# Optimization experiments

Measured on AMD Instinct MI355X. Metric: run time of the kernel, lower is better.

The kernel has to match this reference:

```python
import jax, jax.numpy as jnp
import numpy as np

N = 50000      # nodes
E = 800000     # edges (before self loops)
F_IN = 128     # input feature dim
H = 4          # attention heads
C = 64         # per-head channels (hidden_dim = out_channels = 64)
HC = H * C     # 256, concat output width of each GATv2Conv
G = 32         # number of graphs in the batch
NEG_SLOPE_ATT = 0.2   # GATv2 internal LeakyReLU
NEG_SLOPE_ACT = 0.01  # encoder nn.LeakyReLU() default


def _glorot(key, shape, fan_in):
    return jax.random.normal(key, shape, jnp.float32) * (1.0 / np.sqrt(fan_in))


def setup_inputs() -> dict:
    key = jax.random.key(0)
    ks = jax.random.split(key, 32)
    inp = {}
    inp["x"] = jax.random.normal(ks[0], (N, F_IN), jnp.float32)
    inp["edge_index"] = jax.random.randint(ks[1], (2, E), 0, N, jnp.int32)
    inp["batch"] = jnp.sort(jax.random.randint(ks[2], (N,), 0, G, jnp.int32))
    i = 3
    for li, fin in ((1, F_IN), (2, HC), (3, HC)):
        inp[f"Wl{li}"] = _glorot(ks[i], (HC, fin), fin); i += 1
        inp[f"bl{li}"] = jnp.zeros((HC,), jnp.float32)
        inp[f"Wr{li}"] = _glorot(ks[i], (HC, fin), fin); i += 1
        inp[f"br{li}"] = jnp.zeros((HC,), jnp.float32)
        inp[f"att{li}"] = _glorot(ks[i], (H, C), C); i += 1
        inp[f"bo{li}"] = jnp.zeros((HC,), jnp.float32)
    return inp


def _gatv2_layer(x, src, dst, Wl, bl, Wr, br, att, bo):
    n = x.shape[0]
    xl = (x @ Wl.T + bl).reshape(n, H, C)  # source transform
    xr = (x @ Wr.T + br).reshape(n, H, C)  # target transform
    # per-edge attention logits: a^T LeakyReLU(xl[j] + xr[i])
    e = jax.nn.leaky_relu(xl[src] + xr[dst], negative_slope=NEG_SLOPE_ATT)  # [E', H, C]
    score = jnp.einsum('ehc,hc->eh', e, att)                                # [E', H]
    # segment softmax over incoming edges of each destination node
    m = jax.ops.segment_max(score, dst, num_segments=n)
    p = jnp.exp(score - m[dst])
    s = jax.ops.segment_sum(p, dst, num_segments=n)
    alpha = p / s[dst]
    out = jax.ops.segment_sum(alpha[:, :, None] * xl[src], dst, num_segments=n)
    return out.reshape(n, HC) + bo


def reference(x, edge_index, batch,
              Wl1, bl1, Wr1, br1, att1, bo1,
              Wl2, bl2, Wr2, br2, att2, bo2,
              Wl3, bl3, Wr3, br3, att3, bo3):
    loop = jnp.arange(N, dtype=edge_index.dtype)
    src = jnp.concatenate([edge_index[0], loop])  # add self loops (PyG default)
    dst = jnp.concatenate([edge_index[1], loop])
    h = _gatv2_layer(x, src, dst, Wl1, bl1, Wr1, br1, att1, bo1)
    h = jax.nn.leaky_relu(h, negative_slope=NEG_SLOPE_ACT)
    h = _gatv2_layer(h, src, dst, Wl2, bl2, Wr2, br2, att2, bo2)
    h = jax.nn.leaky_relu(h, negative_slope=NEG_SLOPE_ACT)
    h = _gatv2_layer(h, src, dst, Wl3, bl3, Wr3, br3, att3, bo3)
    # global mean pool over graphs
    sums = jax.ops.segment_sum(h, batch, num_segments=G)
    cnt = jax.ops.segment_sum(jnp.ones((N,), h.dtype), batch, num_segments=G)
    return sums / jnp.maximum(cnt, 1.0)[:, None]
```

## Files before the change

### kernel.cpp

```cpp
#include <hip/hip_runtime.h>

#define HEADS 4
#define CH 64
#define HC 256
#define NGRAPH 32
#define NEG_ATT 0.2f
#define NEG_ACT 0.01f

typedef __attribute__((ext_vector_type(8))) short bf16x8;
typedef __attribute__((ext_vector_type(4))) float f32x4;
typedef __attribute__((ext_vector_type(2))) float f32x2;

typedef __attribute__((address_space(3))) unsigned int lds_u32;
typedef const __attribute__((address_space(1))) unsigned int glob_u32;

__device__ __forceinline__ void gl_lds16(const void* g, void* l) {
  __builtin_amdgcn_global_load_lds((glob_u32*)(uintptr_t)g,
                                   (lds_u32*)(unsigned int)(uintptr_t)l, 16, 0, 0);
}

__device__ __forceinline__ void split2(float a, float b, unsigned& hi, unsigned& lo) {
  unsigned ua = __float_as_uint(a), ub = __float_as_uint(b);
  float la = a - __uint_as_float(ua & 0xFFFF0000u);
  float lb = b - __uint_as_float(ub & 0xFFFF0000u);
  hi = __builtin_amdgcn_perm(ub, ua, 0x07060302u);
  lo = __builtin_amdgcn_perm(__float_as_uint(lb), __float_as_uint(la), 0x07060302u);
}

__device__ __forceinline__ unsigned rtn_bf16(float f) {
  unsigned u = __float_as_uint(f);
  return (u + 0x7FFFu + ((u >> 16) & 1u)) >> 16;
}
__device__ __forceinline__ unsigned rtn_pack2(float a, float b) {
  return (rtn_bf16(b) << 16) | rtn_bf16(a);
}

__global__ __launch_bounds__(256) void convert_x(
    const float* __restrict__ X, unsigned short* __restrict__ xhi,
    unsigned short* __restrict__ xlo, int total4) {
  int g = blockIdx.x * 256 + threadIdx.x;
  if (g >= total4) return;
  float4 v = *(const float4*)&X[(size_t)g * 4];
  uint2 h2, l2;
  split2(v.x, v.y, h2.x, l2.x);
  split2(v.z, v.w, h2.y, l2.y);
  *(uint2*)&xhi[(size_t)g * 4] = h2;
  *(uint2*)&xlo[(size_t)g * 4] = l2;
}

__device__ __forceinline__ void conv_w_one(
    int g, const float* Wl, const float* Wr, int K,
    unsigned short* wfhi, unsigned short* wflo) {
  int lane = g & 63;
  int ct = (g >> 6) & 31;
  int kb = g >> 11;
  int col = ct * 16 + (lane & 15);
  int k = kb * 32 + (lane >> 4) * 8;
  const float* src = (col < HC) ? &Wl[(size_t)col * K + k] : &Wr[(size_t)(col - HC) * K + k];
  float4 v0 = *(const float4*)src;
  float4 v1 = *(const float4*)(src + 4);
  uint4 hq, lq;
  split2(v0.x, v0.y, hq.x, lq.x);
  split2(v0.z, v0.w, hq.y, lq.y);
  split2(v1.x, v1.y, hq.z, lq.z);
  split2(v1.z, v1.w, hq.w, lq.w);
  *(uint4*)&wfhi[(size_t)g * 8] = hq;
  *(uint4*)&wflo[(size_t)g * 8] = lq;
}

__global__ __launch_bounds__(256) void convert_w_all(
    const float* __restrict__ Wl1, const float* __restrict__ Wr1,
    unsigned short* __restrict__ w1hi, unsigned short* __restrict__ w1lo,
    const float* __restrict__ Wl2, const float* __restrict__ Wr2,
    unsigned short* __restrict__ w2hi, unsigned short* __restrict__ w2lo,
    const float* __restrict__ Wl3, const float* __restrict__ Wr3,
    unsigned short* __restrict__ w3hi, unsigned short* __restrict__ w3lo) {
  int g = blockIdx.x * 256 + threadIdx.x;
  if (g < 8192) conv_w_one(g, Wl1, Wr1, 128, w1hi, w1lo);
  else if (g < 8192 + 16384) conv_w_one(g - 8192, Wl2, Wr2, 256, w2hi, w2lo);
  else conv_w_one(g - 8192 - 16384, Wl3, Wr3, 256, w3hi, w3lo);
}

template <int K>
__global__ __launch_bounds__(256) void gemm_fused(
    const unsigned short* __restrict__ xhi, const unsigned short* __restrict__ xlo,
    const unsigned short* __restrict__ wfhi, const unsigned short* __restrict__ wflo,
    const float* __restrict__ bl, const float* __restrict__ br,
    unsigned short* __restrict__ Y1, unsigned short* __restrict__ Y2, int N, int nrb) {
  constexpr int nkb = K >> 5;
  __shared__ unsigned short Ah[2][128][32];
  __shared__ unsigned short Al[2][128][32];

  const int f = blockIdx.x;
  const int rb = (f & 7) + 8 * (f >> 5);
  const int cb = (f >> 3) & 3;
  if (rb >= nrb) return;

  const int tid = threadIdx.x;
  const int wave = tid >> 6;
  const int lane = tid & 63;
  const int quad = lane >> 4;
  const int l16 = lane & 15;
  const int wr = (wave >> 1) * 64;
  const int wc = (wave & 1) * 64;
  const int row0 = rb * 128;
  const int col0 = cb * 128;
  const int ctg0 = cb * 8 + (wave & 1) * 4;

  const int c0 = tid, c1 = tid + 256;
  const int r0g = row0 + (c0 >> 2), r1g = row0 + (c1 >> 2);
  const int ko0 = (c0 & 3) * 8, ko1 = (c1 & 3) * 8;
  const int gr0 = (r0g < N) ? r0g : N - 1;
  const int gr1 = (r1g < N) ? r1g : N - 1;

  f32x4 acc[4][4];
#pragma unroll
  for (int i = 0; i < 4; i++)
#pragma unroll
    for (int j = 0; j < 4; j++) acc[i][j] = (f32x4){0.f, 0.f, 0.f, 0.f};

  {
    size_t ga0 = (size_t)gr0 * K + ko0;
    size_t ga1 = (size_t)gr1 * K + ko1;
    gl_lds16(&xhi[ga0], &Ah[0][c0 >> 2][ko0]);
    gl_lds16(&xlo[ga0], &Al[0][c0 >> 2][ko0]);
    gl_lds16(&xhi[ga1], &Ah[0][c1 >> 2][ko1]);
    gl_lds16(&xlo[ga1], &Al[0][c1 >> 2][ko1]);
  }

#pragma unroll
  for (int kb = 0; kb < nkb; kb++) {
    const int cur = kb & 1, nxt = cur ^ 1;
    bf16x8 bhi[4], blo[4];
#pragma unroll
    for (int j = 0; j < 4; j++) {
      size_t ci = ((size_t)kb * 32 + ctg0 + j) * 64 + lane;
      bhi[j] = *(const bf16x8*)&wfhi[ci * 8];
      blo[j] = *(const bf16x8*)&wflo[ci * 8];
    }
    __syncthreads();
    if (kb + 1 < nkb) {
      int k0 = (kb + 1) * 32;
      size_t ga0 = (size_t)gr0 * K + k0 + ko0;
      size_t ga1 = (size_t)gr1 * K + k0 + ko1;
      gl_lds16(&xhi[ga0], &Ah[nxt][c0 >> 2][ko0]);
      gl_lds16(&xlo[ga0], &Al[nxt][c0 >> 2][ko0]);
      gl_lds16(&xhi[ga1], &Ah[nxt][c1 >> 2][ko1]);
      gl_lds16(&xlo[ga1], &Al[nxt][c1 >> 2][ko1]);
    }
    bf16x8 ahi[4], alo[4];
#pragma unroll
    for (int i = 0; i < 4; i++) {
      ahi[i] = *(const bf16x8*)&Ah[cur][wr + i * 16 + l16][quad * 8];
      alo[i] = *(const bf16x8*)&Al[cur][wr + i * 16 + l16][quad * 8];
    }
#pragma unroll
    for (int i = 0; i < 4; i++)
#pragma unroll
      for (int j = 0; j < 4; j++) {
        acc[i][j] = __builtin_amdgcn_mfma_f32_16x16x32_bf16(ahi[i], bhi[j], acc[i][j], 0, 0, 0);
        acc[i][j] = __builtin_amdgcn_mfma_f32_16x16x32_bf16(ahi[i], blo[j], acc[i][j], 0, 0, 0);
        acc[i][j] = __builtin_amdgcn_mfma_f32_16x16x32_bf16(alo[i], bhi[j], acc[i][j], 0, 0, 0);
      }
  }

#pragma unroll
  for (int j = 0; j < 4; j++) {
    int colg = col0 + wc + j * 16 + l16;
    unsigned short* Yp = (colg < HC) ? Y1 : Y2;
    int cc = (colg < HC) ? colg : colg - HC;
    float bv = (colg < HC) ? bl[cc] : br[cc];
#pragma unroll
    for (int i = 0; i < 4; i++)
#pragma unroll
      for (int r = 0; r < 4; r++) {
        int row = row0 + wr + i * 16 + quad * 4 + r;
        if (row < N)
          Yp[(size_t)row * HC + cc] = (unsigned short)rtn_bf16(acc[i][j][r] + bv);
      }
  }
}

__global__ __launch_bounds__(256) void hist_dst(
    const int* __restrict__ edst, int* __restrict__ counts, int E) {
  int e = blockIdx.x * 256 + threadIdx.x;
  if (e < E) atomicAdd(&counts[edst[e]], 1);
}

__global__ __launch_bounds__(256) void scan_blocks(
    const int* __restrict__ counts, int* __restrict__ row_start,
    int* __restrict__ bsum, int N) {
  __shared__ int tmp[256];
  int t = threadIdx.x;
  int base = blockIdx.x * 1024 + t * 4;
  int v0 = (base     < N) ? counts[base]     + 1 : 0;
  int v1 = (base + 1 < N) ? counts[base + 1] + 1 : 0;
  int v2 = (base + 2 < N) ? counts[base + 2] + 1 : 0;
  int v3 = (base + 3 < N) ? counts[base + 3] + 1 : 0;
  int c1 = v0 + v1, c2 = c1 + v2, tot = c2 + v3;
  tmp[t] = tot;
  __syncthreads();
  for (int off = 1; off < 256; off <<= 1) {
    int add = (t >= off) ? tmp[t - off] : 0;
    __syncthreads();
    tmp[t] += add;
    __syncthreads();
  }
  int excl = tmp[t] - tot;
  if (base     < N) row_start[base + 1] = excl + v0;
  if (base + 1 < N) row_start[base + 2] = excl + c1;
  if (base + 2 < N) row_start[base + 3] = excl + c2;
  if (base + 3 < N) row_start[base + 4] = excl + tot;
  if (t == 255) bsum[blockIdx.x] = tmp[255];
  if (blockIdx.x == 0 && t == 0) row_start[0] = 0;
}

__global__ void scan_tops(int* __restrict__ bsum, int nb) {
  int lane = threadIdx.x;
  int v = (lane < nb) ? bsum[lane] : 0;
  for (int off = 1; off < 64; off <<= 1) {
    int u = __shfl_up(v, off);
    if (lane >= off) v += u;
  }
  if (lane < nb) bsum[lane] = v;
}

__global__ __launch_bounds__(256) void scan_add(
    int* __restrict__ row_start, const int* __restrict__ bsum, int N) {
  int off = bsum[blockIdx.x];
  int i = (blockIdx.x + 1) * 1024 + threadIdx.x * 4;
#pragma unroll
  for (int k = 0; k < 4; k++)
    if (i + k < N) row_start[i + k + 1] += off;
}

__global__ __launch_bounds__(256) void csr_init(
    const int* __restrict__ row_start, int* __restrict__ fill_pos,
    int* __restrict__ csr_src, int N) {
  int i = blockIdx.x * 256 + threadIdx.x;
  if (i < N) {
    int p = row_start[i];
    csr_src[p] = i << 9;
    fill_pos[i] = p + 1;
  }
}

__global__ __launch_bounds__(256) void csr_scatter(
    const int* __restrict__ esrc, const int* __restrict__ edst,
    int* __restrict__ fill_pos, int* __restrict__ csr_src, int E) {
  int e = blockIdx.x * 256 + threadIdx.x;
  if (e < E) {
    int p = atomicAdd(&fill_pos[edst[e]], 1);
    csr_src[p] = esrc[e] << 9;
  }
}

__device__ __forceinline__ void unpk(uint2 q, f32x2& v01, f32x2& v23) {
  v01.x = __uint_as_float(q.x << 16);
  v01.y = __uint_as_float(q.x & 0xFFFF0000u);
  v23.x = __uint_as_float(q.y << 16);
  v23.y = __uint_as_float(q.y & 0xFFFF0000u);
}

__device__ __forceinline__ float edot(f32x2 l01, f32x2 l23, f32x2 r01, f32x2 r23,
                                      f32x2 a01, f32x2 a23) {
  f32x2 t01 = l01 + r01, t23 = l23 + r23;
  f32x2 u01 = t01 * NEG_ATT, u23 = t23 * NEG_ATT;
  t01.x = fmaxf(t01.x, u01.x); t01.y = fmaxf(t01.y, u01.y);
  t23.x = fmaxf(t23.x, u23.x); t23.y = fmaxf(t23.y, u23.y);
  f32x2 dv = t01 * a01 + t23 * a23;
  float d = dv.x + dv.y;
  d += __shfl_xor(d, 1);
  d += __shfl_xor(d, 2);
  d += __shfl_xor(d, 4);
  d += __shfl_xor(d, 8);
  return d;
}

__global__ __launch_bounds__(256) void gat_fused(
    const unsigned short* __restrict__ xl, const unsigned short* __restrict__ xr,
    const int* __restrict__ row_start, const int* __restrict__ csr_soff,
    const float* __restrict__ att, const float* __restrict__ bo,
    unsigned short* __restrict__ ohi, unsigned short* __restrict__ olo,
    int N, int mode) {
  int dst = (blockIdx.x * 256 + threadIdx.x) >> 6;
  int lane = threadIdx.x & 63;
  if (dst >= N) return;
  int h = lane >> 4;
  int off = h * CH + (lane & 15) * 4;
  const int loff = off * 2;
  const char* xlc = (const char*)xl;
  f32x2 a01 = *(const f32x2*)&att[off];
  f32x2 a23 = *(const f32x2*)&att[off + 2];
  f32x2 r01, r23;
  unpk(*(const uint2*)&xr[(size_t)dst * HC + off], r01, r23);
  f32x2 o01 = {0.f, 0.f}, o23 = {0.f, 0.f};
  float s = 0.f;
  int p = row_start[dst];
  int end = row_start[dst + 1];
  for (; p + 4 <= end; p += 4) {
    int b0 = csr_soff[p + 0] + loff, b1 = csr_soff[p + 1] + loff;
    int b2 = csr_soff[p + 2] + loff, b3 = csr_soff[p + 3] + loff;
    uint2 q0 = *(const uint2*)(xlc + b0);
    uint2 q1 = *(const uint2*)(xlc + b1);
    uint2 q2 = *(const uint2*)(xlc + b2);
    uint2 q3 = *(const uint2*)(xlc + b3);
    f32x2 l0a, l0b, l1a, l1b, l2a, l2b, l3a, l3b;
    unpk(q0, l0a, l0b);
    unpk(q1, l1a, l1b);
    unpk(q2, l2a, l2b);
    unpk(q3, l3a, l3b);
    float e0 = __expf(edot(l0a, l0b, r01, r23, a01, a23));
    float e1 = __expf(edot(l1a, l1b, r01, r23, a01, a23));
    float e2 = __expf(edot(l2a, l2b, r01, r23, a01, a23));
    float e3 = __expf(edot(l3a, l3b, r01, r23, a01, a23));
    s += (e0 + e1) + (e2 + e3);
    o01 = l0a * e0 + o01;
    o01 = l1a * e1 + o01;
    o01 = l2a * e2 + o01;
    o01 = l3a * e3 + o01;
    o23 = l0b * e0 + o23;
    o23 = l1b * e1 + o23;
    o23 = l2b * e2 + o23;
    o23 = l3b * e3 + o23;
  }
  for (; p < end; p++) {
    int b0 = csr_soff[p] + loff;
    uint2 q0 = *(const uint2*)(xlc + b0);
    f32x2 la, lb;
    unpk(q0, la, lb);
    float pe = __expf(edot(la, lb, r01, r23, a01, a23));
    s += pe;
    o01 = la * pe + o01;
    o23 = lb * pe + o23;
  }
  float inv = 1.f / s;
  f32x2 b01 = *(const f32x2*)&bo[off];
  f32x2 b23 = *(const f32x2*)&bo[off + 2];
  f32x2 res01 = o01 * inv + b01;
  f32x2 res23 = o23 * inv + b23;
  if (mode == 1) {
    f32x2 v01 = res01 * NEG_ACT, v23 = res23 * NEG_ACT;
    res01.x = fmaxf(res01.x, v01.x); res01.y = fmaxf(res01.y, v01.y);
    res23.x = fmaxf(res23.x, v23.x); res23.y = fmaxf(res23.y, v23.y);
    uint2 h2, l2;
    split2(res01.x, res01.y, h2.x, l2.x);
    split2(res23.x, res23.y, h2.y, l2.y);
    *(uint2*)&ohi[(size_t)dst * HC + off] = h2;
    *(uint2*)&olo[(size_t)dst * HC + off] = l2;
  } else {
    uint2 pk;
    pk.x = rtn_pack2(res01.x, res01.y);
    pk.y = rtn_pack2(res23.x, res23.y);
    *(uint2*)&ohi[(size_t)dst * HC + off] = pk;
  }
}

__global__ __launch_bounds__(256) void pool_partial(
    const unsigned short* __restrict__ h3, const int* __restrict__ batch,
    float* __restrict__ out, int* __restrict__ cnt, int N) {
  __shared__ float part[NGRAPH][HC];
  __shared__ int bsh[256];
  __shared__ int cpart[NGRAPH];
  int j = threadIdx.x;
#pragma unroll
  for (int g = 0; g < NGRAPH; g++) part[g][j] = 0.f;
  if (j < NGRAPH) cpart[j] = 0;
  int n0 = blockIdx.x * 256;
  int nend = min(n0 + 256, N);
  int nj = n0 + j;
  bsh[j] = (nj < N) ? batch[nj] : 0;
  __syncthreads();
  if (nj < nend) atomicAdd(&cpart[bsh[j]], 1);
  for (int n = n0; n < nend; n++) {
    int g = bsh[n - n0];
    unsigned q = h3[(size_t)n * HC + j];
    part[g][j] += __uint_as_float(q << 16);
  }
  __syncthreads();
#pragma unroll
  for (int g = 0; g < NGRAPH; g++) {
    float v = part[g][j];
    if (v != 0.f) atomicAdd(&out[g * HC + j], v);
  }
  if (j < NGRAPH && cpart[j] > 0) atomicAdd(&cnt[j], cpart[j]);
}

__global__ __launch_bounds__(256) void pool_final(
    float* __restrict__ out, const int* __restrict__ cnt) {
  int g = blockIdx.x;
  int j = threadIdx.x;
  float c = (float)max(cnt[g], 1);
  out[g * HC + j] /= c;
}

extern "C" void kernel_launch(void* const* d_in, const int* in_sizes, int n_in,
                              void* d_out, int out_size, void* d_ws, size_t ws_size,
                              hipStream_t stream) {
  const float* x = (const float*)d_in[0];
  const int* ei = (const int*)d_in[1];
  const int* batch = (const int*)d_in[2];
  const int N = in_sizes[2];
  const int E = in_sizes[1] / 2;
  const int Etot = E + N;

  const float* Wl[3] = {(const float*)d_in[3], (const float*)d_in[9], (const float*)d_in[15]};
  const float* bl[3] = {(const float*)d_in[4], (const float*)d_in[10], (const float*)d_in[16]};
  const float* Wr[3] = {(const float*)d_in[5], (const float*)d_in[11], (const float*)d_in[17]};
  const float* br[3] = {(const float*)d_in[6], (const float*)d_in[12], (const float*)d_in[18]};
  const float* att[3] = {(const float*)d_in[7], (const float*)d_in[13], (const float*)d_in[19]};
  const float* bo[3] = {(const float*)d_in[8], (const float*)d_in[14], (const float*)d_in[20]};

  float* B0 = (float*)d_ws;
  float* B1 = B0 + (size_t)N * HC;
  float* B2 = B1 + (size_t)N * HC;
  unsigned short* w1hi = (unsigned short*)(B2 + (size_t)N * HC);
  unsigned short* w1lo = w1hi + 512 * 128;
  unsigned short* w2hi = w1lo + 512 * 128;
  unsigned short* w2lo = w2hi + 512 * 256;
  unsigned short* w3hi = w2lo + 512 * 256;
  unsigned short* w3lo = w3hi + 512 * 256;
  int* counts = (int*)(w3lo + 512 * 256);
  int* row_start = counts + N;
  int* bsum = row_start + N + 1;
  int* fill_pos = bsum + 64;
  int* csr_src = fill_pos + N;
  int* cnt = csr_src + Etot;

  unsigned short* xlB = (unsigned short*)B1;
  unsigned short* xrB = (unsigned short*)B2;
  unsigned short* xhiL1 = (unsigned short*)B0;
  unsigned short* xloL1 = xhiL1 + (size_t)N * 128;
  unsigned short* xhiL = (unsigned short*)B0;
  unsigned short* xloL = xhiL + (size_t)N * HC;
  unsigned short* h3B = (unsigned short*)B0;

  const int* esrc = ei;
  const int* edst = ei + E;

  convert_x<<<(N * 128 / 4 + 255) / 256, 256, 0, stream>>>(x, xhiL1, xloL1, N * 128 / 4);
  convert_w_all<<<(8192 + 16384 + 16384) / 256, 256, 0, stream>>>(
      Wl[0], Wr[0], w1hi, w1lo, Wl[1], Wr[1], w2hi, w2lo, Wl[2], Wr[2], w3hi, w3lo);

  const int nscan = (N + 1023) / 1024;
  (void)hipMemsetAsync(counts, 0, (size_t)N * sizeof(int), stream);
  hist_dst<<<(E + 255) / 256, 256, 0, stream>>>(edst, counts, E);
  scan_blocks<<<nscan, 256, 0, stream>>>(counts, row_start, bsum, N);
  scan_tops<<<1, 64, 0, stream>>>(bsum, nscan);
  scan_add<<<nscan - 1, 256, 0, stream>>>(row_start, bsum, N);
  csr_init<<<(N + 255) / 256, 256, 0, stream>>>(row_start, fill_pos, csr_src, N);
  csr_scatter<<<(E + 255) / 256, 256, 0, stream>>>(esrc, edst, fill_pos, csr_src, E);

  const int nrb = (N + 127) / 128;
  const int gblocks = ((nrb + 7) / 8) * 32;
  const int fblocks = (N * 64 + 255) / 256;

  gemm_fused<128><<<gblocks, 256, 0, stream>>>(xhiL1, xloL1, w1hi, w1lo, bl[0], br[0], xlB, xrB, N, nrb);
  gat_fused<<<fblocks, 256, 0, stream>>>(xlB, xrB, row_start, csr_src, att[0], bo[0],
                                         xhiL, xloL, N, 1);
  gemm_fused<256><<<gblocks, 256, 0, stream>>>(xhiL, xloL, w2hi, w2lo, bl[1], br[1], xlB, xrB, N, nrb);
  gat_fused<<<fblocks, 256, 0, stream>>>(xlB, xrB, row_start, csr_src, att[1], bo[1],
                                         xhiL, xloL, N, 1);
  gemm_fused<256><<<gblocks, 256, 0, stream>>>(xhiL, xloL, w3hi, w3lo, bl[2], br[2], xlB, xrB, N, nrb);
  gat_fused<<<fblocks, 256, 0, stream>>>(xlB, xrB, row_start, csr_src, att[2], bo[2],
                                         h3B, nullptr, N, 2);

  (void)hipMemsetAsync(d_out, 0, NGRAPH * HC * sizeof(float), stream);
  (void)hipMemsetAsync(cnt, 0, NGRAPH * sizeof(int), stream);
  pool_partial<<<(N + 255) / 256, 256, 0, stream>>>(h3B, batch, (float*)d_out, cnt, N);
  pool_final<<<NGRAPH, 256, 0, stream>>>((float*)d_out, cnt);
}
```

Measured before the change: 648.0 us.

## Split wavefront into two half-waves processing alternate edges with 16-byte gathers

The per-destination aggregation kernel now maps each lane to 8 channels instead of 4. The two 32-lane halves of a wavefront each take alternate incoming edges, and their partial softmax sums and outputs are combined with a cross-half shuffle at the end. Gathers of source features widen to 16-byte loads, and the per-head dot-product reduction needs one fewer shuffle step. The tail loop handles edge parity with predication, and only half the lanes write results.

```diff
diff --git a/kernel.cpp b/kernel.cpp
--- a/kernel.cpp
+++ b/kernel.cpp
@@ -255,25 +255,32 @@
   }
 }
 
-__device__ __forceinline__ void unpk(uint2 q, f32x2& v01, f32x2& v23) {
-  v01.x = __uint_as_float(q.x << 16);
-  v01.y = __uint_as_float(q.x & 0xFFFF0000u);
-  v23.x = __uint_as_float(q.y << 16);
-  v23.y = __uint_as_float(q.y & 0xFFFF0000u);
-}
-
-__device__ __forceinline__ float edot(f32x2 l01, f32x2 l23, f32x2 r01, f32x2 r23,
-                                      f32x2 a01, f32x2 a23) {
-  f32x2 t01 = l01 + r01, t23 = l23 + r23;
-  f32x2 u01 = t01 * NEG_ATT, u23 = t23 * NEG_ATT;
-  t01.x = fmaxf(t01.x, u01.x); t01.y = fmaxf(t01.y, u01.y);
-  t23.x = fmaxf(t23.x, u23.x); t23.y = fmaxf(t23.y, u23.y);
-  f32x2 dv = t01 * a01 + t23 * a23;
+__device__ __forceinline__ void unpk8(uint4 q, f32x2& v0, f32x2& v1, f32x2& v2, f32x2& v3) {
+  v0.x = __uint_as_float(q.x << 16); v0.y = __uint_as_float(q.x & 0xFFFF0000u);
+  v1.x = __uint_as_float(q.y << 16); v1.y = __uint_as_float(q.y & 0xFFFF0000u);
+  v2.x = __uint_as_float(q.z << 16); v2.y = __uint_as_float(q.z & 0xFFFF0000u);
+  v3.x = __uint_as_float(q.w << 16); v3.y = __uint_as_float(q.w & 0xFFFF0000u);
+}
+
+__device__ __forceinline__ float edge8(uint4 q,
+    f32x2 r0, f32x2 r1, f32x2 r2, f32x2 r3,
+    f32x2 a0, f32x2 a1, f32x2 a2, f32x2 a3,
+    f32x2& l0, f32x2& l1, f32x2& l2, f32x2& l3) {
+  unpk8(q, l0, l1, l2, l3);
+  f32x2 t0 = l0 + r0, t1 = l1 + r1, t2 = l2 + r2, t3 = l3 + r3;
+  f32x2 u0 = t0 * NEG_ATT, u1 = t1 * NEG_ATT, u2 = t2 * NEG_ATT, u3 = t3 * NEG_ATT;
+  t0.x = fmaxf(t0.x, u0.x); t0.y = fmaxf(t0.y, u0.y);
+  t1.x = fmaxf(t1.x, u1.x); t1.y = fmaxf(t1.y, u1.y);
+  t2.x = fmaxf(t2.x, u2.x); t2.y = fmaxf(t2.y, u2.y);
+  t3.x = fmaxf(t3.x, u3.x); t3.y = fmaxf(t3.y, u3.y);
+  f32x2 dv = t0 * a0;
+  dv = t1 * a1 + dv;
+  dv = t2 * a2 + dv;
+  dv = t3 * a3 + dv;
   float d = dv.x + dv.y;
   d += __shfl_xor(d, 1);
   d += __shfl_xor(d, 2);
   d += __shfl_xor(d, 4);
-  d += __shfl_xor(d, 8);
   return d;
 }
 
@@ -286,73 +293,92 @@
   int dst = (blockIdx.x * 256 + threadIdx.x) >> 6;
   int lane = threadIdx.x & 63;
   if (dst >= N) return;
-  int h = lane >> 4;
-  int off = h * CH + (lane & 15) * 4;
-  const int loff = off * 2;
+  const int slot = lane >> 5;
+  const int c8 = (lane & 31) * 8;
+  const int loff = c8 * 2;
   const char* xlc = (const char*)xl;
-  f32x2 a01 = *(const f32x2*)&att[off];
-  f32x2 a23 = *(const f32x2*)&att[off + 2];
-  f32x2 r01, r23;
-  unpk(*(const uint2*)&xr[(size_t)dst * HC + off], r01, r23);
-  f32x2 o01 = {0.f, 0.f}, o23 = {0.f, 0.f};
+
+  f32x2 a0 = *(const f32x2*)&att[c8 + 0];
+  f32x2 a1 = *(const f32x2*)&att[c8 + 2];
+  f32x2 a2 = *(const f32x2*)&att[c8 + 4];
+  f32x2 a3 = *(const f32x2*)&att[c8 + 6];
+
+  uint4 qr = *(const uint4*)((const char*)xr + (size_t)dst * 512 + loff);
+  f32x2 r0, r1, r2, r3;
+  unpk8(qr, r0, r1, r2, r3);
+
+  f32x2 o0 = {0.f, 0.f}, o1 = {0.f, 0.f}, o2 = {0.f, 0.f}, o3 = {0.f, 0.f};
   float s = 0.f;
   int p = row_start[dst];
-  int end = row_start[dst + 1];
+  const int end = row_start[dst + 1];
+
   for (; p + 4 <= end; p += 4) {
-    int b0 = csr_soff[p + 0] + loff, b1 = csr_soff[p + 1] + loff;
-    int b2 = csr_soff[p + 2] + loff, b3 = csr_soff[p + 3] + loff;
-    uint2 q0 = *(const uint2*)(xlc + b0);
-    uint2 q1 = *(const uint2*)(xlc + b1);
-    uint2 q2 = *(const uint2*)(xlc + b2);
-    uint2 q3 = *(const uint2*)(xlc + b3);
-    f32x2 l0a, l0b, l1a, l1b, l2a, l2b, l3a, l3b;
-    unpk(q0, l0a, l0b);
-    unpk(q1, l1a, l1b);
-    unpk(q2, l2a, l2b);
-    unpk(q3, l3a, l3b);
-    float e0 = __expf(edot(l0a, l0b, r01, r23, a01, a23));
-    float e1 = __expf(edot(l1a, l1b, r01, r23, a01, a23));
-    float e2 = __expf(edot(l2a, l2b, r01, r23, a01, a23));
-    float e3 = __expf(edot(l3a, l3b, r01, r23, a01, a23));
-    s += (e0 + e1) + (e2 + e3);
-    o01 = l0a * e0 + o01;
-    o01 = l1a * e1 + o01;
-    o01 = l2a * e2 + o01;
-    o01 = l3a * e3 + o01;
-    o23 = l0b * e0 + o23;
-    o23 = l1b * e1 + o23;
-    o23 = l2b * e2 + o23;
-    o23 = l3b * e3 + o23;
-  }
-  for (; p < end; p++) {
-    int b0 = csr_soff[p] + loff;
-    uint2 q0 = *(const uint2*)(xlc + b0);
-    f32x2 la, lb;
-    unpk(q0, la, lb);
-    float pe = __expf(edot(la, lb, r01, r23, a01, a23));
+    int iA = csr_soff[p + slot];
+    int iB = csr_soff[p + 2 + slot];
+    uint4 qA = *(const uint4*)(xlc + iA + loff);
+    uint4 qB = *(const uint4*)(xlc + iB + loff);
+    f32x2 lA0, lA1, lA2, lA3, lB0, lB1, lB2, lB3;
+    float dA = edge8(qA, r0, r1, r2, r3, a0, a1, a2, a3, lA0, lA1, lA2, lA3);
+    float dB = edge8(qB, r0, r1, r2, r3, a0, a1, a2, a3, lB0, lB1, lB2, lB3);
+    float eA = __expf(dA);
+    float eB = __expf(dB);
+    s += eA + eB;
+    o0 = lA0 * eA + o0; o0 = lB0 * eB + o0;
+    o1 = lA1 * eA + o1; o1 = lB1 * eB + o1;
+    o2 = lA2 * eA + o2; o2 = lB2 * eB + o2;
+    o3 = lA3 * eA + o3; o3 = lB3 * eB + o3;
+  }
+  for (; p < end; p += 2) {
+    int i = p + slot;
+    bool vld = i < end;
+    int ii = vld ? i : end - 1;
+    uint4 q = *(const uint4*)(xlc + csr_soff[ii] + loff);
+    f32x2 l0, l1, l2, l3;
+    float d = edge8(q, r0, r1, r2, r3, a0, a1, a2, a3, l0, l1, l2, l3);
+    float pe = vld ? __expf(d) : 0.f;
     s += pe;
-    o01 = la * pe + o01;
-    o23 = lb * pe + o23;
-  }
+    o0 = l0 * pe + o0;
+    o1 = l1 * pe + o1;
+    o2 = l2 * pe + o2;
+    o3 = l3 * pe + o3;
+  }
+
+  s += __shfl_xor(s, 32);
+  o0.x += __shfl_xor(o0.x, 32); o0.y += __shfl_xor(o0.y, 32);
+  o1.x += __shfl_xor(o1.x, 32); o1.y += __shfl_xor(o1.y, 32);
+  o2.x += __shfl_xor(o2.x, 32); o2.y += __shfl_xor(o2.y, 32);
+  o3.x += __shfl_xor(o3.x, 32); o3.y += __shfl_xor(o3.y, 32);
+
+  if (slot != 0) return;
   float inv = 1.f / s;
-  f32x2 b01 = *(const f32x2*)&bo[off];
-  f32x2 b23 = *(const f32x2*)&bo[off + 2];
-  f32x2 res01 = o01 * inv + b01;
-  f32x2 res23 = o23 * inv + b23;
+  f32x2 b0 = *(const f32x2*)&bo[c8 + 0];
+  f32x2 b1 = *(const f32x2*)&bo[c8 + 2];
+  f32x2 b2 = *(const f32x2*)&bo[c8 + 4];
+  f32x2 b3 = *(const f32x2*)&bo[c8 + 6];
+  f32x2 s0 = o0 * inv + b0;
+  f32x2 s1 = o1 * inv + b1;
+  f32x2 s2 = o2 * inv + b2;
+  f32x2 s3 = o3 * inv + b3;
   if (mode == 1) {
-    f32x2 v01 = res01 * NEG_ACT, v23 = res23 * NEG_ACT;
-    res01.x = fmaxf(res01.x, v01.x); res01.y = fmaxf(res01.y, v01.y);
-    res23.x = fmaxf(res23.x, v23.x); res23.y = fmaxf(res23.y, v23.y);
-    uint2 h2, l2;
-    split2(res01.x, res01.y, h2.x, l2.x);
-    split2(res23.x, res23.y, h2.y, l2.y);
-    *(uint2*)&ohi[(size_t)dst * HC + off] = h2;
-    *(uint2*)&olo[(size_t)dst * HC + off] = l2;
+    f32x2 w0 = s0 * NEG_ACT, w1 = s1 * NEG_ACT, w2 = s2 * NEG_ACT, w3 = s3 * NEG_ACT;
+    s0.x = fmaxf(s0.x, w0.x); s0.y = fmaxf(s0.y, w0.y);
+    s1.x = fmaxf(s1.x, w1.x); s1.y = fmaxf(s1.y, w1.y);
+    s2.x = fmaxf(s2.x, w2.x); s2.y = fmaxf(s2.y, w2.y);
+    s3.x = fmaxf(s3.x, w3.x); s3.y = fmaxf(s3.y, w3.y);
+    uint4 hq, lq;
+    split2(s0.x, s0.y, hq.x, lq.x);
+    split2(s1.x, s1.y, hq.y, lq.y);
+    split2(s2.x, s2.y, hq.z, lq.z);
+    split2(s3.x, s3.y, hq.w, lq.w);
+    *(uint4*)&ohi[(size_t)dst * HC + c8] = hq;
+    *(uint4*)&olo[(size_t)dst * HC + c8] = lq;
   } else {
-    uint2 pk;
-    pk.x = rtn_pack2(res01.x, res01.y);
-    pk.y = rtn_pack2(res23.x, res23.y);
-    *(uint2*)&ohi[(size_t)dst * HC + off] = pk;
+    uint4 pk;
+    pk.x = rtn_pack2(s0.x, s0.y);
+    pk.y = rtn_pack2(s1.x, s1.y);
+    pk.z = rtn_pack2(s2.x, s2.y);
+    pk.w = rtn_pack2(s3.x, s3.y);
+    *(uint4*)&ohi[(size_t)dst * HC + c8] = pk;
   }
 }
 
```

Result: no change. 643.1 us (-0.7%).
